# Kernel optimization log

Measured on AMD Instinct MI355X. Metric: run time of the kernel, lower is better.

## Reference

```python
import jax, jax.numpy as jnp
import numpy as np

T, BS, N = 256, 512, 2048
FUDGE = 1e-4


def setup_inputs() -> dict:
    key = jax.random.key(0)
    ks = jax.random.split(key, 6)
    f32 = jnp.float32
    return {
        "noises": jax.random.normal(ks[0], (T, BS), f32) * 0.1,  # per-step process noise [T, bs]
        "ys": jax.random.normal(ks[1], (T,), f32),               # per-step scalar targets
        "qs": jax.random.normal(ks[2], (T,), f32),               # per-step scalar context input
        "z_biases": jax.random.normal(ks[3], (N,), f32),         # random-feature bias directions
        "w_in": jax.random.normal(ks[4], (N,), f32),             # random input weights
        "w_inq": jax.random.normal(ks[5], (N,), f32),            # random q-input weights
        # scalar learned params (legacy init values)
        "log_learning_rate": jnp.array(-6.0, f32),
        "log_learning_rate_decay": jnp.array(0.0, f32),
        "sigma_b": jnp.array(0.1, f32),
        "output_scale": jnp.array(1.0, f32),
        "u_feedback_scale": jnp.array(1.0, f32),
        "log_weight_decay": jnp.array(-0.001, f32),
        "q_scale": jnp.array(1.0, f32),
        "tauqlpf_m1": jnp.array(-1.0, f32),
        "tauylpf_m1": jnp.array(-1.0, f32),
    }


def _forward(noises, ys, qs, z_biases, w_in, w_inq,
             log_learning_rate, log_learning_rate_decay, sigma_b,
             output_scale, u_feedback_scale, log_weight_decay, q_scale,
             tauqlpf_m1, tauylpf_m1):
    bs = noises.shape[1]
    n = w_in.shape[0]
    softplus = lambda v: jnp.log1p(jnp.exp(v))
    biases = sigma_b * z_biases                    # [n]
    lr0 = jnp.exp(log_learning_rate)               # scalar
    tauq = 1.0 + softplus(tauqlpf_m1)
    tauy = 1.0 + softplus(tauylpf_m1)
    wd = jnp.exp(log_weight_decay)                 # tie_lr_weight_decay=False -> scalar decay
    lr_decay_rate = jnp.exp(log_learning_rate_decay)

    def step(carry, inp):
        w_out, u, e, lr_mult, qlp, ylp = carry
        y, noise_x, q = inp
        qlp = (1.0 - tauq) * qlp + tauq * q
        q_in = w_inq * (q_scale * qlp)             # [n]
        x = u * u_feedback_scale + e + noise_x     # noise injected at node 'x'; [bs]
        h = jax.nn.relu(biases[None, :] + x[:, None] * w_in[None, :] + q_in[None, :])  # [bs, n]
        u = jnp.einsum('kj,kj->k', w_out, h)       # [bs]
        a_mean = output_scale * u                  # [bs]
        # y observed every step (no None/NaN branch)
        ylp = (1.0 - tauy) * ylp + tauy * y
        e = ylp - u                                # [bs]
        lr = lr0 * lr_mult                         # [bs]
        dw = e[:, None] * h * lr[:, None]          # [bs, n]
        w_out = w_out + dw
        norms = jnp.sqrt(FUDGE + jnp.sum(dw * dw, axis=1))
        lr_mult = lr_mult * jnp.exp(-lr_decay_rate * norms)
        w_out = wd * w_out
        return (w_out, u, e, lr_mult, qlp, ylp), a_mean

    init = (jnp.zeros((bs, n), noises.dtype),
            jnp.zeros((bs,), noises.dtype),
            jnp.zeros((bs,), noises.dtype),
            jnp.ones((bs,), noises.dtype),
            jnp.zeros((), noises.dtype),
            jnp.zeros((), noises.dtype))
    _, a_means = jax.lax.scan(step, init, (ys, noises, qs))
    return a_means  # [T, bs]


def reference(noises, ys, qs, z_biases, w_in, w_inq,
              log_learning_rate, log_learning_rate_decay, sigma_b,
              output_scale, u_feedback_scale, log_weight_decay, q_scale,
              tauqlpf_m1, tauylpf_m1):
    return _forward(noises, ys, qs, z_biases, w_in, w_inq,
                    log_learning_rate, log_learning_rate_decay, sigma_b,
                    output_scale, u_feedback_scale, log_weight_decay, q_scale,
                    tauqlpf_m1, tauylpf_m1)
```

## Files before the change

kernel.cpp:

```cpp
#include <hip/hip_runtime.h>
#include <math.h>
#include <stdint.h>

#define T_STEPS 256
#define BS      512
#define N       2048
#define BLOCK   256
#define FUDGE   1e-4f

__global__ __launch_bounds__(BLOCK, 2)
void legacy_elbo_scan_kernel(
    const float* __restrict__ noises,
    const float* __restrict__ ys,
    const float* __restrict__ qs,
    const float* __restrict__ z_biases,
    const float* __restrict__ w_in,
    const float* __restrict__ w_inq,
    const float* __restrict__ p_llr,
    const float* __restrict__ p_llrd,
    const float* __restrict__ p_sigb,
    const float* __restrict__ p_oscale,
    const float* __restrict__ p_ufs,
    const float* __restrict__ p_lwd,
    const float* __restrict__ p_qscale,
    const float* __restrict__ p_tauq,
    const float* __restrict__ p_tauy,
    float* __restrict__ out)
{
    const int tid = threadIdx.x;
    const int blk = blockIdx.x;

    __shared__ float red_lds[16];
    if (tid < 16) red_lds[tid] = 0.0f;
    __syncthreads();

    const float sigb    = p_sigb[0];
    const float lr0     = expf(p_llr[0]);
    const float lr_decay= expf(p_llrd[0]);
    const float wd      = expf(p_lwd[0]);
    const float rwd     = 1.0f / wd;
    const float tauq    = 1.0f + log1pf(expf(p_tauq[0]));
    const float tauy    = 1.0f + log1pf(expf(p_tauy[0]));
    const float omtq    = 1.0f - tauq;
    const float omty    = 1.0f - tauy;
    const float qscale  = p_qscale[0];
    const float ufs     = p_ufs[0];
    const float oscale  = p_oscale[0];
    const float nld2    = -lr_decay * 1.4426950408889634f;

    const float* nzp = noises + blk;
    const int    ovo = blk * 4;

    asm volatile(
        "v_lshrrev_b32 v3, 6, %[vtid]\n\t"
        "v_lshlrev_b32 v4, 3, v3\n\t"
        "v_and_b32 v7, 63, %[vtid]\n\t"
        "v_cmp_eq_u32 vcc, 63, v7\n\t"
        "s_mov_b64 s[74:75], vcc\n\t"
        "v_cmp_eq_u32 vcc, 0, %[vtid]\n\t"
        "s_mov_b64 s[76:77], vcc\n\t"
        "v_mov_b32 v5, 0\n\t"
        "v_lshlrev_b32 v1, 4, %[vtid]\n\t"
        "v_add_u32 v2, 0x1000, v1\n\t"
        "global_load_dwordx4 v[40:43], v1, %[pzb]\n\t"
        "global_load_dwordx4 v[44:47], v2, %[pzb]\n\t"
        "global_load_dwordx4 v[48:51], v1, %[pwi]\n\t"
        "global_load_dwordx4 v[52:55], v2, %[pwi]\n\t"
        "global_load_dwordx4 v[56:59], v1, %[pwq]\n\t"
        "global_load_dwordx4 v[60:63], v2, %[pwq]\n\t"
        "s_waitcnt vmcnt(0)\n\t"
        "v_mul_f32 v40, %[osg], v40\n\t"  "v_mul_f32 v41, %[osg], v41\n\t"
        "v_mul_f32 v42, %[osg], v42\n\t"  "v_mul_f32 v43, %[osg], v43\n\t"
        "v_mul_f32 v44, %[osg], v44\n\t"  "v_mul_f32 v45, %[osg], v45\n\t"
        "v_mul_f32 v46, %[osg], v46\n\t"  "v_mul_f32 v47, %[osg], v47\n\t"
        "v_mov_b32 v64, 0\n\t" "v_mov_b32 v65, 0\n\t" "v_mov_b32 v66, 0\n\t" "v_mov_b32 v67, 0\n\t"
        "v_mov_b32 v68, 0\n\t" "v_mov_b32 v69, 0\n\t" "v_mov_b32 v70, 0\n\t" "v_mov_b32 v71, 0\n\t"
        "v_mov_b32 v20, 0\n\t" "v_mov_b32 v21, 0\n\t" "v_mov_b32 v22, 0\n\t" "v_mov_b32 v23, 0\n\t"
        "v_mov_b32 v24, 1.0\n\t" "v_mov_b32 v25, 1.0\n\t" "v_mov_b32 v26, 1.0\n\t"
        "v_mov_b32 v6, %[ovo]\n\t"
        "s_mov_b32 s60, 0\n\t"
        "s_mov_b32 s61, 12\n\t"
        "s_mov_b32 s62, 0x1800\n\t"
        "s_load_dword s66, %[pys], 0x0\n\t"
        "s_load_dword s67, %[pqs], 0x0\n\t"
        "s_load_dword s68, %[pnz], 0x0\n\t"
        "s_load_dword s69, %[pys], 0x4\n\t"
        "s_load_dword s70, %[pqs], 0x4\n\t"
        "s_load_dword s71, %[pnz], 0x800\n\t"
        "s_load_dword s50, %[pys], 0x8\n\t"
        "s_load_dword s51, %[pqs], 0x8\n\t"
        "s_load_dword s52, %[pnz], 0x1000\n\t"
        "s_waitcnt lgkmcnt(0)\n\t"
        "Lelbo3:\n\t"
        "v_mov_b32 v30, s67\n\t"
        "v_mul_f32 v20, %[omq], v20\n\t"
        "v_fmac_f32 v20, %[otq], v30\n\t"
        "v_mul_f32 v10, %[oq], v20\n\t"
        "v_mov_b32 v11, v10\n\t"
        "v_mov_b32 v8, s68\n\t"
        "v_add_f32 v8, v23, v8\n\t"
        "v_fmac_f32 v8, %[ouf], v22\n\t"
        "v_mov_b32 v9, v8\n\t"
        "v_mov_b32 v12, 0\n\t" "v_mov_b32 v13, 0\n\t"
        "v_mov_b32 v14, 0\n\t" "v_mov_b32 v15, 0\n\t"
        "v_pk_fma_f32 v[72:73], v[10:11], v[56:57], v[40:41]\n\t"
        "v_pk_fma_f32 v[74:75], v[10:11], v[58:59], v[42:43]\n\t"
        "v_pk_fma_f32 v[76:77], v[10:11], v[60:61], v[44:45]\n\t"
        "v_pk_fma_f32 v[78:79], v[10:11], v[62:63], v[46:47]\n\t"
        "v_pk_fma_f32 v[72:73], v[8:9], v[48:49], v[72:73]\n\t"
        "v_pk_fma_f32 v[74:75], v[8:9], v[50:51], v[74:75]\n\t"
        "v_pk_fma_f32 v[76:77], v[8:9], v[52:53], v[76:77]\n\t"
        "v_pk_fma_f32 v[78:79], v[8:9], v[54:55], v[78:79]\n\t"
        "v_max_f32 v72, 0, v72\n\t" "v_max_f32 v73, 0, v73\n\t"
        "v_max_f32 v74, 0, v74\n\t" "v_max_f32 v75, 0, v75\n\t"
        "v_max_f32 v76, 0, v76\n\t" "v_max_f32 v77, 0, v77\n\t"
        "v_max_f32 v78, 0, v78\n\t" "v_max_f32 v79, 0, v79\n\t"
        "v_pk_fma_f32 v[12:13], v[64:65], v[72:73], v[12:13]\n\t"
        "v_pk_fma_f32 v[14:15], v[72:73], v[72:73], v[14:15]\n\t"
        "v_pk_fma_f32 v[12:13], v[66:67], v[74:75], v[12:13]\n\t"
        "v_pk_fma_f32 v[14:15], v[74:75], v[74:75], v[14:15]\n\t"
        "v_pk_fma_f32 v[12:13], v[68:69], v[76:77], v[12:13]\n\t"
        "v_pk_fma_f32 v[14:15], v[76:77], v[76:77], v[14:15]\n\t"
        "v_pk_fma_f32 v[12:13], v[70:71], v[78:79], v[12:13]\n\t"
        "v_pk_fma_f32 v[14:15], v[78:79], v[78:79], v[14:15]\n\t"
        "v_add_f32 v12, v12, v13\n\t"
        "v_add_f32 v14, v14, v15\n\t"
        "s_nop 1\n\t"
        "v_mov_b32_dpp v30, v12 row_shr:1 row_mask:0xf bank_mask:0xf\n\t"
        "v_mov_b32_dpp v31, v14 row_shr:1 row_mask:0xf bank_mask:0xf\n\t"
        "v_add_f32 v12, v12, v30\n\t"
        "v_add_f32 v14, v14, v31\n\t"
        "s_nop 0\n\t"
        "v_mov_b32_dpp v30, v12 row_shr:2 row_mask:0xf bank_mask:0xf\n\t"
        "v_mov_b32_dpp v31, v14 row_shr:2 row_mask:0xf bank_mask:0xf\n\t"
        "v_add_f32 v12, v12, v30\n\t"
        "v_add_f32 v14, v14, v31\n\t"
        "s_nop 0\n\t"
        "v_mov_b32_dpp v30, v12 row_shr:4 row_mask:0xf bank_mask:0xf\n\t"
        "v_mov_b32_dpp v31, v14 row_shr:4 row_mask:0xf bank_mask:0xf\n\t"
        "v_add_f32 v12, v12, v30\n\t"
        "v_add_f32 v14, v14, v31\n\t"
        "s_nop 0\n\t"
        "v_mov_b32_dpp v30, v12 row_shr:8 row_mask:0xf bank_mask:0xf\n\t"
        "v_mov_b32_dpp v31, v14 row_shr:8 row_mask:0xf bank_mask:0xf\n\t"
        "v_add_f32 v12, v12, v30\n\t"
        "v_add_f32 v14, v14, v31\n\t"
        "s_nop 0\n\t"
        "v_mov_b32_dpp v30, v12 row_bcast:15 row_mask:0xf bank_mask:0xf\n\t"
        "v_mov_b32_dpp v31, v14 row_bcast:15 row_mask:0xf bank_mask:0xf\n\t"
        "v_add_f32 v12, v12, v30\n\t"
        "v_add_f32 v14, v14, v31\n\t"
        "s_nop 0\n\t"
        "v_mov_b32_dpp v30, v12 row_bcast:31 row_mask:0xf bank_mask:0xf\n\t"
        "v_mov_b32_dpp v31, v14 row_bcast:31 row_mask:0xf bank_mask:0xf\n\t"
        "v_add_f32 v12, v12, v30\n\t"
        "v_add_f32 v14, v14, v31\n\t"
        "s_nop 1\n\t"
        "s_and_saveexec_b64 s[72:73], s[74:75]\n\t"
        "ds_write2_b32 v4, v12, v14 offset0:0 offset1:1\n\t"
        "s_mov_b64 exec, s[72:73]\n\t"
        "s_waitcnt lgkmcnt(0)\n\t"
        "s_barrier\n\t"
        "ds_read_b128 v[32:35], v5\n\t"
        "ds_read_b128 v[36:39], v5 offset:16\n\t"
        "v_mov_b32 v30, s66\n\t"
        "v_mul_f32 v21, %[omy], v21\n\t"
        "v_fmac_f32 v21, %[oty], v30\n\t"
        "v_xor_b32 v4, 32, v4\n\t"
        "v_xor_b32 v5, 32, v5\n\t"
        "s_mov_b32 s66, s69\n\t"
        "s_mov_b32 s67, s70\n\t"
        "s_mov_b32 s68, s71\n\t"
        "s_mov_b32 s69, s50\n\t"
        "s_mov_b32 s70, s51\n\t"
        "s_mov_b32 s71, s52\n\t"
        "s_add_u32 s60, s60, 1\n\t"
        "s_waitcnt lgkmcnt(0)\n\t"
        "v_pk_add_f32 v[32:33], v[32:33], v[34:35]\n\t"
        "v_pk_add_f32 v[36:37], v[36:37], v[38:39]\n\t"
        "v_pk_add_f32 v[32:33], v[32:33], v[36:37]\n\t"
        "v_mul_f32 v22, v25, v32\n\t"
        "v_mul_f32 v30, %[oos], v22\n\t"
        "s_and_saveexec_b64 s[72:73], s[76:77]\n\t"
        "global_store_dword v6, v30, %[pou]\n\t"
        "s_mov_b64 exec, s[72:73]\n\t"
        "v_add_u32 v6, 0x800, v6\n\t"
        "v_sub_f32 v23, v21, v22\n\t"
        "v_mul_f32 v27, %[olr], v23\n\t"
        "v_mul_f32 v27, v27, v24\n\t"
        "v_mul_f32 v28, v27, v26\n\t"
        "v_mov_b32 v29, v28\n\t"
        "s_load_dword s50, %[pys], s61\n\t"
        "s_load_dword s51, %[pqs], s61\n\t"
        "s_load_dword s52, %[pnz], s62\n\t"
        "s_add_u32 s61, s61, 4\n\t"
        "s_min_u32 s61, s61, 0x3fc\n\t"
        "s_add_u32 s62, s62, 0x800\n\t"
        "s_min_u32 s62, s62, 0x7f800\n\t"
        "v_pk_fma_f32 v[64:65], v[28:29], v[72:73], v[64:65]\n\t"
        "v_pk_fma_f32 v[66:67], v[28:29], v[74:75], v[66:67]\n\t"
        "v_pk_fma_f32 v[68:69], v[28:29], v[76:77], v[68:69]\n\t"
        "v_pk_fma_f32 v[70:71], v[28:29], v[78:79], v[70:71]\n\t"
        "v_mul_f32 v30, v27, v27\n\t"
        "v_mul_f32 v30, v33, v30\n\t"
        "v_add_f32 v30, 0x38d1b717, v30\n\t"
        "v_sqrt_f32 v30, v30\n\t"
        "s_nop 1\n\t"
        "v_mul_f32 v30, %[ond], v30\n\t"
        "v_exp_f32 v30, v30\n\t"
        "s_nop 1\n\t"
        "v_mul_f32 v24, v24, v30\n\t"
        "v_mul_f32 v25, %[owd], v25\n\t"
        "v_mul_f32 v26, %[orw], v26\n\t"
        "s_cmp_lt_u32 s60, 0x100\n\t"
        "s_cbranch_scc1 Lelbo3\n\t"
        "s_waitcnt vmcnt(0)\n\t"
        :
        : [pys]"s"(ys), [pqs]"s"(qs), [pnz]"s"(nzp), [pou]"s"(out),
          [pzb]"s"(z_biases), [pwi]"s"(w_in), [pwq]"s"(w_inq),
          [vtid]"v"(tid), [ovo]"v"(ovo),
          [osg]"v"(sigb), [otq]"v"(tauq), [omq]"v"(omtq),
          [oty]"v"(tauy), [omy]"v"(omty), [oq]"v"(qscale),
          [ouf]"v"(ufs), [olr]"v"(lr0), [owd]"v"(wd), [orw]"v"(rwd),
          [oos]"v"(oscale), [ond]"v"(nld2)
        : "memory", "scc", "vcc",
          "s50","s51","s52",
          "s60","s61","s62","s63","s64","s65","s66","s67","s68","s69",
          "s70","s71","s72","s73","s74","s75","s76","s77",
          "v1","v2","v3","v4","v5","v6","v7","v8","v9","v10","v11",
          "v12","v13","v14","v15","v16","v17","v18","v19","v20","v21",
          "v22","v23","v24","v25","v26","v27","v28","v29","v30","v31",
          "v32","v33","v34","v35","v36","v37","v38","v39","v40","v41",
          "v42","v43","v44","v45","v46","v47","v48","v49","v50","v51",
          "v52","v53","v54","v55","v56","v57","v58","v59","v60","v61",
          "v62","v63","v64","v65","v66","v67","v68","v69","v70","v71",
          "v72","v73","v74","v75","v76","v77","v78","v79"
    );
}

extern "C" void kernel_launch(void* const* d_in, const int* in_sizes, int n_in,
                              void* d_out, int out_size, void* d_ws, size_t ws_size,
                              hipStream_t stream) {
    (void)in_sizes; (void)n_in; (void)d_ws; (void)ws_size; (void)out_size;
    const float* noises   = (const float*)d_in[0];
    const float* ys       = (const float*)d_in[1];
    const float* qs       = (const float*)d_in[2];
    const float* z_biases = (const float*)d_in[3];
    const float* w_in     = (const float*)d_in[4];
    const float* w_inq    = (const float*)d_in[5];
    const float* llr      = (const float*)d_in[6];
    const float* llrd     = (const float*)d_in[7];
    const float* sigb     = (const float*)d_in[8];
    const float* oscale   = (const float*)d_in[9];
    const float* ufs      = (const float*)d_in[10];
    const float* lwd      = (const float*)d_in[11];
    const float* qscale   = (const float*)d_in[12];
    const float* tauq     = (const float*)d_in[13];
    const float* tauy     = (const float*)d_in[14];
    float* out = (float*)d_out;

    hipLaunchKernelGGL(legacy_elbo_scan_kernel, dim3(BS), dim3(BLOCK), 64, stream,
                       noises, ys, qs, z_biases, w_in, w_inq,
                       llr, llrd, sigb, oscale, ufs, lwd, qscale, tauq, tauy,
                       out);
}
```

Baseline: 189.2 us.

## Process two batch rows per block, sharing barriers and q-input precompute

Each block now handles two batch elements, so the grid halves to 256 blocks. The per-step w_in/z_bias/w_inq registers and the q-dependent pre-activation are shared across both rows. Reductions for both rows are interleaved in a single DPP chain and one LDS exchange, which halves barriers per element and gives more independent instructions to hide latency. The qlp/ylp and x updates are precomputed and pipelined off the critical path. In exchange it uses more VGPRs and only 256 blocks, which may underfill a 256-CU device.

```diff
diff --git a/kernel.cpp b/kernel.cpp
--- a/kernel.cpp
+++ b/kernel.cpp
@@ -8,7 +8,7 @@
 #define BLOCK   256
 #define FUDGE   1e-4f
 
-__global__ __launch_bounds__(BLOCK, 2)
+__global__ __launch_bounds__(BLOCK)
 void legacy_elbo_scan_kernel(
     const float* __restrict__ noises,
     const float* __restrict__ ys,
@@ -30,8 +30,8 @@
     const int tid = threadIdx.x;
     const int blk = blockIdx.x;
 
-    __shared__ float red_lds[16];
-    if (tid < 16) red_lds[tid] = 0.0f;
+    __shared__ float red_lds[32];
+    if (tid < 32) red_lds[tid] = 0.0f;
     __syncthreads();
 
     const float sigb    = p_sigb[0];
@@ -44,16 +44,16 @@
     const float omtq    = 1.0f - tauq;
     const float omty    = 1.0f - tauy;
     const float qscale  = p_qscale[0];
-    const float ufs     = p_ufs[0];
+    const float ufsm1   = p_ufs[0] - 1.0f;
     const float oscale  = p_oscale[0];
     const float nld2    = -lr_decay * 1.4426950408889634f;
 
-    const float* nzp = noises + blk;
-    const int    ovo = blk * 4;
+    const float* nzp = noises + 2 * blk;
+    const int    ovo = blk * 8;
 
     asm volatile(
         "v_lshrrev_b32 v3, 6, %[vtid]\n\t"
-        "v_lshlrev_b32 v4, 3, v3\n\t"
+        "v_lshlrev_b32 v4, 4, v3\n\t"
         "v_and_b32 v7, 63, %[vtid]\n\t"
         "v_cmp_eq_u32 vcc, 63, v7\n\t"
         "s_mov_b64 s[74:75], vcc\n\t"
@@ -62,171 +62,256 @@
         "v_mov_b32 v5, 0\n\t"
         "v_lshlrev_b32 v1, 4, %[vtid]\n\t"
         "v_add_u32 v2, 0x1000, v1\n\t"
-        "global_load_dwordx4 v[40:43], v1, %[pzb]\n\t"
-        "global_load_dwordx4 v[44:47], v2, %[pzb]\n\t"
-        "global_load_dwordx4 v[48:51], v1, %[pwi]\n\t"
-        "global_load_dwordx4 v[52:55], v2, %[pwi]\n\t"
-        "global_load_dwordx4 v[56:59], v1, %[pwq]\n\t"
-        "global_load_dwordx4 v[60:63], v2, %[pwq]\n\t"
-        "s_waitcnt vmcnt(0)\n\t"
-        "v_mul_f32 v40, %[osg], v40\n\t"  "v_mul_f32 v41, %[osg], v41\n\t"
-        "v_mul_f32 v42, %[osg], v42\n\t"  "v_mul_f32 v43, %[osg], v43\n\t"
-        "v_mul_f32 v44, %[osg], v44\n\t"  "v_mul_f32 v45, %[osg], v45\n\t"
-        "v_mul_f32 v46, %[osg], v46\n\t"  "v_mul_f32 v47, %[osg], v47\n\t"
+        "global_load_dwordx4 v[56:59], v1, %[pzb]\n\t"
+        "global_load_dwordx4 v[60:63], v2, %[pzb]\n\t"
+        "global_load_dwordx4 v[40:43], v1, %[pwi]\n\t"
+        "global_load_dwordx4 v[44:47], v2, %[pwi]\n\t"
+        "global_load_dwordx4 v[48:51], v1, %[pwq]\n\t"
+        "global_load_dwordx4 v[52:55], v2, %[pwq]\n\t"
+        "s_load_dword s66, %[pys], 0x0\n\t"
+        "s_load_dword s67, %[pqs], 0x0\n\t"
+        "s_load_dwordx2 s[68:69], %[pnz], 0x0\n\t"
+        "s_load_dword s70, %[pys], 0x4\n\t"
+        "s_load_dword s71, %[pqs], 0x4\n\t"
+        "s_load_dwordx2 s[54:55], %[pnz], 0x800\n\t"
+        "s_load_dword s50, %[pys], 0x8\n\t"
+        "s_load_dword s51, %[pqs], 0x8\n\t"
+        "s_load_dwordx2 s[52:53], %[pnz], 0x1000\n\t"
+        "s_mov_b32 s61, 12\n\t"
+        "s_mov_b32 s62, 0x1800\n\t"
+        "s_mov_b32 s60, 0\n\t"
+        "s_waitcnt vmcnt(0) lgkmcnt(0)\n\t"
+        "v_mul_f32 v56, %[osg], v56\n\t" "v_mul_f32 v57, %[osg], v57\n\t"
+        "v_mul_f32 v58, %[osg], v58\n\t" "v_mul_f32 v59, %[osg], v59\n\t"
+        "v_mul_f32 v60, %[osg], v60\n\t" "v_mul_f32 v61, %[osg], v61\n\t"
+        "v_mul_f32 v62, %[osg], v62\n\t" "v_mul_f32 v63, %[osg], v63\n\t"
         "v_mov_b32 v64, 0\n\t" "v_mov_b32 v65, 0\n\t" "v_mov_b32 v66, 0\n\t" "v_mov_b32 v67, 0\n\t"
         "v_mov_b32 v68, 0\n\t" "v_mov_b32 v69, 0\n\t" "v_mov_b32 v70, 0\n\t" "v_mov_b32 v71, 0\n\t"
-        "v_mov_b32 v20, 0\n\t" "v_mov_b32 v21, 0\n\t" "v_mov_b32 v22, 0\n\t" "v_mov_b32 v23, 0\n\t"
-        "v_mov_b32 v24, 1.0\n\t" "v_mov_b32 v25, 1.0\n\t" "v_mov_b32 v26, 1.0\n\t"
+        "v_mov_b32 v96, 0\n\t" "v_mov_b32 v97, 0\n\t" "v_mov_b32 v98, 0\n\t" "v_mov_b32 v99, 0\n\t"
+        "v_mov_b32 v100, 0\n\t" "v_mov_b32 v101, 0\n\t" "v_mov_b32 v102, 0\n\t" "v_mov_b32 v103, 0\n\t"
+        "v_mov_b32 v105, 0\n\t"
+        "v_mov_b32 v108, 1.0\n\t" "v_mov_b32 v109, 1.0\n\t"
+        "v_mov_b32 v110, 1.0\n\t" "v_mov_b32 v111, 1.0\n\t"
         "v_mov_b32 v6, %[ovo]\n\t"
-        "s_mov_b32 s60, 0\n\t"
-        "s_mov_b32 s61, 12\n\t"
-        "s_mov_b32 s62, 0x1800\n\t"
-        "s_load_dword s66, %[pys], 0x0\n\t"
-        "s_load_dword s67, %[pqs], 0x0\n\t"
-        "s_load_dword s68, %[pnz], 0x0\n\t"
-        "s_load_dword s69, %[pys], 0x4\n\t"
-        "s_load_dword s70, %[pqs], 0x4\n\t"
-        "s_load_dword s71, %[pnz], 0x800\n\t"
-        "s_load_dword s50, %[pys], 0x8\n\t"
-        "s_load_dword s51, %[pqs], 0x8\n\t"
-        "s_load_dword s52, %[pnz], 0x1000\n\t"
-        "s_waitcnt lgkmcnt(0)\n\t"
-        "Lelbo3:\n\t"
-        "v_mov_b32 v30, s67\n\t"
-        "v_mul_f32 v20, %[omq], v20\n\t"
-        "v_fmac_f32 v20, %[otq], v30\n\t"
-        "v_mul_f32 v10, %[oq], v20\n\t"
-        "v_mov_b32 v11, v10\n\t"
-        "v_mov_b32 v8, s68\n\t"
-        "v_add_f32 v8, v23, v8\n\t"
-        "v_fmac_f32 v8, %[ouf], v22\n\t"
-        "v_mov_b32 v9, v8\n\t"
-        "v_mov_b32 v12, 0\n\t" "v_mov_b32 v13, 0\n\t"
-        "v_mov_b32 v14, 0\n\t" "v_mov_b32 v15, 0\n\t"
-        "v_pk_fma_f32 v[72:73], v[10:11], v[56:57], v[40:41]\n\t"
-        "v_pk_fma_f32 v[74:75], v[10:11], v[58:59], v[42:43]\n\t"
-        "v_pk_fma_f32 v[76:77], v[10:11], v[60:61], v[44:45]\n\t"
-        "v_pk_fma_f32 v[78:79], v[10:11], v[62:63], v[46:47]\n\t"
-        "v_pk_fma_f32 v[72:73], v[8:9], v[48:49], v[72:73]\n\t"
-        "v_pk_fma_f32 v[74:75], v[8:9], v[50:51], v[74:75]\n\t"
-        "v_pk_fma_f32 v[76:77], v[8:9], v[52:53], v[76:77]\n\t"
-        "v_pk_fma_f32 v[78:79], v[8:9], v[54:55], v[78:79]\n\t"
-        "v_max_f32 v72, 0, v72\n\t" "v_max_f32 v73, 0, v73\n\t"
-        "v_max_f32 v74, 0, v74\n\t" "v_max_f32 v75, 0, v75\n\t"
-        "v_max_f32 v76, 0, v76\n\t" "v_max_f32 v77, 0, v77\n\t"
-        "v_max_f32 v78, 0, v78\n\t" "v_max_f32 v79, 0, v79\n\t"
-        "v_pk_fma_f32 v[12:13], v[64:65], v[72:73], v[12:13]\n\t"
-        "v_pk_fma_f32 v[14:15], v[72:73], v[72:73], v[14:15]\n\t"
-        "v_pk_fma_f32 v[12:13], v[66:67], v[74:75], v[12:13]\n\t"
-        "v_pk_fma_f32 v[14:15], v[74:75], v[74:75], v[14:15]\n\t"
-        "v_pk_fma_f32 v[12:13], v[68:69], v[76:77], v[12:13]\n\t"
-        "v_pk_fma_f32 v[14:15], v[76:77], v[76:77], v[14:15]\n\t"
-        "v_pk_fma_f32 v[12:13], v[70:71], v[78:79], v[12:13]\n\t"
-        "v_pk_fma_f32 v[14:15], v[78:79], v[78:79], v[14:15]\n\t"
-        "v_add_f32 v12, v12, v13\n\t"
-        "v_add_f32 v14, v14, v15\n\t"
+        "v_mul_f32 v104, s67, %[otq]\n\t"
+        "v_mul_f32 v12, v104, %[oq]\n\t"
+        "v_mov_b32 v13, v12\n\t"
+        "v_pk_fma_f32 v[80:81], v[12:13], v[48:49], v[56:57]\n\t"
+        "v_pk_fma_f32 v[82:83], v[12:13], v[50:51], v[58:59]\n\t"
+        "v_pk_fma_f32 v[84:85], v[12:13], v[52:53], v[60:61]\n\t"
+        "v_pk_fma_f32 v[86:87], v[12:13], v[54:55], v[62:63]\n\t"
+        "v_mov_b32 v8, s68\n\t"  "v_mov_b32 v9, v8\n\t"
+        "v_mov_b32 v10, s69\n\t" "v_mov_b32 v11, v10\n\t"
+        "Lelbo5:\n\t"
+        "v_pk_fma_f32 v[72:73], v[8:9], v[40:41], v[80:81]\n\t"
+        "v_pk_fma_f32 v[88:89], v[10:11], v[40:41], v[80:81]\n\t"
+        "v_pk_fma_f32 v[74:75], v[8:9], v[42:43], v[82:83]\n\t"
+        "v_pk_fma_f32 v[90:91], v[10:11], v[42:43], v[82:83]\n\t"
+        "v_pk_fma_f32 v[76:77], v[8:9], v[44:45], v[84:85]\n\t"
+        "v_pk_fma_f32 v[92:93], v[10:11], v[44:45], v[84:85]\n\t"
+        "v_pk_fma_f32 v[78:79], v[8:9], v[46:47], v[86:87]\n\t"
+        "v_pk_fma_f32 v[94:95], v[10:11], v[46:47], v[86:87]\n\t"
+        "v_max_f32 v72, 0, v72\n\t" "v_max_f32 v88, 0, v88\n\t"
+        "v_max_f32 v73, 0, v73\n\t" "v_max_f32 v89, 0, v89\n\t"
+        "v_max_f32 v74, 0, v74\n\t" "v_max_f32 v90, 0, v90\n\t"
+        "v_max_f32 v75, 0, v75\n\t" "v_max_f32 v91, 0, v91\n\t"
+        "v_max_f32 v76, 0, v76\n\t" "v_max_f32 v92, 0, v92\n\t"
+        "v_max_f32 v77, 0, v77\n\t" "v_max_f32 v93, 0, v93\n\t"
+        "v_max_f32 v78, 0, v78\n\t" "v_max_f32 v94, 0, v94\n\t"
+        "v_max_f32 v79, 0, v79\n\t" "v_max_f32 v95, 0, v95\n\t"
+        "v_pk_mul_f32 v[16:17], v[64:65], v[72:73]\n\t"
+        "v_pk_mul_f32 v[24:25], v[96:97], v[88:89]\n\t"
+        "v_pk_mul_f32 v[18:19], v[66:67], v[74:75]\n\t"
+        "v_pk_mul_f32 v[26:27], v[98:99], v[90:91]\n\t"
+        "v_pk_mul_f32 v[20:21], v[68:69], v[76:77]\n\t"
+        "v_pk_mul_f32 v[28:29], v[100:101], v[92:93]\n\t"
+        "v_pk_mul_f32 v[22:23], v[70:71], v[78:79]\n\t"
+        "v_pk_mul_f32 v[30:31], v[102:103], v[94:95]\n\t"
+        "v_pk_add_f32 v[16:17], v[16:17], v[18:19]\n\t"
+        "v_pk_add_f32 v[24:25], v[24:25], v[26:27]\n\t"
+        "v_pk_add_f32 v[20:21], v[20:21], v[22:23]\n\t"
+        "v_pk_add_f32 v[28:29], v[28:29], v[30:31]\n\t"
+        "v_pk_add_f32 v[16:17], v[16:17], v[20:21]\n\t"
+        "v_pk_add_f32 v[24:25], v[24:25], v[28:29]\n\t"
+        "v_add_f32 v16, v16, v17\n\t"
+        "v_add_f32 v24, v24, v25\n\t"
+        "v_pk_mul_f32 v[18:19], v[72:73], v[72:73]\n\t"
+        "v_pk_mul_f32 v[26:27], v[88:89], v[88:89]\n\t"
+        "v_pk_mul_f32 v[20:21], v[74:75], v[74:75]\n\t"
+        "v_pk_mul_f32 v[28:29], v[90:91], v[90:91]\n\t"
+        "v_pk_mul_f32 v[22:23], v[76:77], v[76:77]\n\t"
+        "v_pk_mul_f32 v[30:31], v[92:93], v[92:93]\n\t"
+        "v_pk_mul_f32 v[36:37], v[78:79], v[78:79]\n\t"
+        "v_pk_mul_f32 v[38:39], v[94:95], v[94:95]\n\t"
+        "v_pk_add_f32 v[18:19], v[18:19], v[20:21]\n\t"
+        "v_pk_add_f32 v[26:27], v[26:27], v[28:29]\n\t"
+        "v_pk_add_f32 v[22:23], v[22:23], v[36:37]\n\t"
+        "v_pk_add_f32 v[30:31], v[30:31], v[38:39]\n\t"
+        "v_pk_add_f32 v[18:19], v[18:19], v[22:23]\n\t"
+        "v_pk_add_f32 v[26:27], v[26:27], v[30:31]\n\t"
+        "v_add_f32 v18, v18, v19\n\t"
+        "v_add_f32 v26, v26, v27\n\t"
         "s_nop 1\n\t"
-        "v_mov_b32_dpp v30, v12 row_shr:1 row_mask:0xf bank_mask:0xf\n\t"
-        "v_mov_b32_dpp v31, v14 row_shr:1 row_mask:0xf bank_mask:0xf\n\t"
-        "v_add_f32 v12, v12, v30\n\t"
-        "v_add_f32 v14, v14, v31\n\t"
-        "s_nop 0\n\t"
-        "v_mov_b32_dpp v30, v12 row_shr:2 row_mask:0xf bank_mask:0xf\n\t"
-        "v_mov_b32_dpp v31, v14 row_shr:2 row_mask:0xf bank_mask:0xf\n\t"
-        "v_add_f32 v12, v12, v30\n\t"
-        "v_add_f32 v14, v14, v31\n\t"
-        "s_nop 0\n\t"
-        "v_mov_b32_dpp v30, v12 row_shr:4 row_mask:0xf bank_mask:0xf\n\t"
-        "v_mov_b32_dpp v31, v14 row_shr:4 row_mask:0xf bank_mask:0xf\n\t"
-        "v_add_f32 v12, v12, v30\n\t"
-        "v_add_f32 v14, v14, v31\n\t"
-        "s_nop 0\n\t"
-        "v_mov_b32_dpp v30, v12 row_shr:8 row_mask:0xf bank_mask:0xf\n\t"
-        "v_mov_b32_dpp v31, v14 row_shr:8 row_mask:0xf bank_mask:0xf\n\t"
-        "v_add_f32 v12, v12, v30\n\t"
-        "v_add_f32 v14, v14, v31\n\t"
-        "s_nop 0\n\t"
-        "v_mov_b32_dpp v30, v12 row_bcast:15 row_mask:0xf bank_mask:0xf\n\t"
-        "v_mov_b32_dpp v31, v14 row_bcast:15 row_mask:0xf bank_mask:0xf\n\t"
-        "v_add_f32 v12, v12, v30\n\t"
-        "v_add_f32 v14, v14, v31\n\t"
-        "s_nop 0\n\t"
-        "v_mov_b32_dpp v30, v12 row_bcast:31 row_mask:0xf bank_mask:0xf\n\t"
-        "v_mov_b32_dpp v31, v14 row_bcast:31 row_mask:0xf bank_mask:0xf\n\t"
-        "v_add_f32 v12, v12, v30\n\t"
-        "v_add_f32 v14, v14, v31\n\t"
+        "v_mov_b32_dpp v32, v16 row_shr:1 row_mask:0xf bank_mask:0xf\n\t"
+        "v_mov_b32_dpp v33, v18 row_shr:1 row_mask:0xf bank_mask:0xf\n\t"
+        "v_mov_b32_dpp v34, v24 row_shr:1 row_mask:0xf bank_mask:0xf\n\t"
+        "v_mov_b32_dpp v35, v26 row_shr:1 row_mask:0xf bank_mask:0xf\n\t"
+        "v_add_f32 v16, v16, v32\n\t"
+        "v_add_f32 v18, v18, v33\n\t"
+        "v_add_f32 v24, v24, v34\n\t"
+        "v_add_f32 v26, v26, v35\n\t"
+        "v_mov_b32_dpp v32, v16 row_shr:2 row_mask:0xf bank_mask:0xf\n\t"
+        "v_mov_b32_dpp v33, v18 row_shr:2 row_mask:0xf bank_mask:0xf\n\t"
+        "v_mov_b32_dpp v34, v24 row_shr:2 row_mask:0xf bank_mask:0xf\n\t"
+        "v_mov_b32_dpp v35, v26 row_shr:2 row_mask:0xf bank_mask:0xf\n\t"
+        "v_add_f32 v16, v16, v32\n\t"
+        "v_add_f32 v18, v18, v33\n\t"
+        "v_add_f32 v24, v24, v34\n\t"
+        "v_add_f32 v26, v26, v35\n\t"
+        "v_mov_b32_dpp v32, v16 row_shr:4 row_mask:0xf bank_mask:0xf\n\t"
+        "v_mov_b32_dpp v33, v18 row_shr:4 row_mask:0xf bank_mask:0xf\n\t"
+        "v_mov_b32_dpp v34, v24 row_shr:4 row_mask:0xf bank_mask:0xf\n\t"
+        "v_mov_b32_dpp v35, v26 row_shr:4 row_mask:0xf bank_mask:0xf\n\t"
+        "v_add_f32 v16, v16, v32\n\t"
+        "v_add_f32 v18, v18, v33\n\t"
+        "v_add_f32 v24, v24, v34\n\t"
+        "v_add_f32 v26, v26, v35\n\t"
+        "v_mov_b32_dpp v32, v16 row_shr:8 row_mask:0xf bank_mask:0xf\n\t"
+        "v_mov_b32_dpp v33, v18 row_shr:8 row_mask:0xf bank_mask:0xf\n\t"
+        "v_mov_b32_dpp v34, v24 row_shr:8 row_mask:0xf bank_mask:0xf\n\t"
+        "v_mov_b32_dpp v35, v26 row_shr:8 row_mask:0xf bank_mask:0xf\n\t"
+        "v_add_f32 v16, v16, v32\n\t"
+        "v_add_f32 v18, v18, v33\n\t"
+        "v_add_f32 v24, v24, v34\n\t"
+        "v_add_f32 v26, v26, v35\n\t"
+        "v_mov_b32_dpp v32, v16 row_bcast:15 row_mask:0xf bank_mask:0xf\n\t"
+        "v_mov_b32_dpp v33, v18 row_bcast:15 row_mask:0xf bank_mask:0xf\n\t"
+        "v_mov_b32_dpp v34, v24 row_bcast:15 row_mask:0xf bank_mask:0xf\n\t"
+        "v_mov_b32_dpp v35, v26 row_bcast:15 row_mask:0xf bank_mask:0xf\n\t"
+        "v_add_f32 v16, v16, v32\n\t"
+        "v_add_f32 v18, v18, v33\n\t"
+        "v_add_f32 v24, v24, v34\n\t"
+        "v_add_f32 v26, v26, v35\n\t"
+        "v_mov_b32_dpp v32, v16 row_bcast:31 row_mask:0xf bank_mask:0xf\n\t"
+        "v_mov_b32_dpp v33, v18 row_bcast:31 row_mask:0xf bank_mask:0xf\n\t"
+        "v_mov_b32_dpp v34, v24 row_bcast:31 row_mask:0xf bank_mask:0xf\n\t"
+        "v_mov_b32_dpp v35, v26 row_bcast:31 row_mask:0xf bank_mask:0xf\n\t"
+        "v_add_f32 v16, v16, v32\n\t"
+        "v_add_f32 v18, v18, v33\n\t"
+        "v_add_f32 v24, v24, v34\n\t"
+        "v_add_f32 v26, v26, v35\n\t"
         "s_nop 1\n\t"
+        "v_mov_b32 v36, v16\n\t"
+        "v_mov_b32 v37, v18\n\t"
+        "v_mov_b32 v38, v24\n\t"
+        "v_mov_b32 v39, v26\n\t"
         "s_and_saveexec_b64 s[72:73], s[74:75]\n\t"
-        "ds_write2_b32 v4, v12, v14 offset0:0 offset1:1\n\t"
+        "ds_write_b128 v4, v[36:39]\n\t"
         "s_mov_b64 exec, s[72:73]\n\t"
         "s_waitcnt lgkmcnt(0)\n\t"
         "s_barrier\n\t"
-        "ds_read_b128 v[32:35], v5\n\t"
-        "ds_read_b128 v[36:39], v5 offset:16\n\t"
-        "v_mov_b32 v30, s66\n\t"
-        "v_mul_f32 v21, %[omy], v21\n\t"
-        "v_fmac_f32 v21, %[oty], v30\n\t"
-        "v_xor_b32 v4, 32, v4\n\t"
-        "v_xor_b32 v5, 32, v5\n\t"
-        "s_mov_b32 s66, s69\n\t"
-        "s_mov_b32 s67, s70\n\t"
-        "s_mov_b32 s68, s71\n\t"
-        "s_mov_b32 s69, s50\n\t"
-        "s_mov_b32 s70, s51\n\t"
-        "s_mov_b32 s71, s52\n\t"
+        "ds_read_b128 v[16:19], v5\n\t"
+        "ds_read_b128 v[20:23], v5 offset:16\n\t"
+        "ds_read_b128 v[24:27], v5 offset:32\n\t"
+        "ds_read_b128 v[28:31], v5 offset:48\n\t"
+        "v_mul_f32 v104, %[omq], v104\n\t"
+        "v_fmac_f32 v104, s71, %[otq]\n\t"
+        "v_mul_f32 v12, v104, %[oq]\n\t"
+        "v_mov_b32 v13, v12\n\t"
+        "v_pk_fma_f32 v[80:81], v[12:13], v[48:49], v[56:57]\n\t"
+        "v_pk_fma_f32 v[82:83], v[12:13], v[50:51], v[58:59]\n\t"
+        "v_pk_fma_f32 v[84:85], v[12:13], v[52:53], v[60:61]\n\t"
+        "v_pk_fma_f32 v[86:87], v[12:13], v[54:55], v[62:63]\n\t"
+        "v_mul_f32 v105, %[omy], v105\n\t"
+        "v_fmac_f32 v105, s66, %[oty]\n\t"
+        "v_add_f32 v112, s54, v105\n\t"
+        "v_add_f32 v113, s55, v105\n\t"
+        "v_mul_f32 v114, %[olr], v108\n\t"
+        "v_mul_f32 v115, %[olr], v109\n\t"
+        "v_xor_b32 v4, 64, v4\n\t"
+        "v_xor_b32 v5, 64, v5\n\t"
+        "s_mov_b32 s66, s70\n\t"
+        "s_mov_b32 s67, s71\n\t"
+        "s_mov_b32 s68, s54\n\t"
+        "s_mov_b32 s69, s55\n\t"
+        "s_mov_b32 s70, s50\n\t"
+        "s_mov_b32 s71, s51\n\t"
+        "s_mov_b32 s54, s52\n\t"
+        "s_mov_b32 s55, s53\n\t"
         "s_add_u32 s60, s60, 1\n\t"
         "s_waitcnt lgkmcnt(0)\n\t"
-        "v_pk_add_f32 v[32:33], v[32:33], v[34:35]\n\t"
-        "v_pk_add_f32 v[36:37], v[36:37], v[38:39]\n\t"
-        "v_pk_add_f32 v[32:33], v[32:33], v[36:37]\n\t"
-        "v_mul_f32 v22, v25, v32\n\t"
-        "v_mul_f32 v30, %[oos], v22\n\t"
-        "s_and_saveexec_b64 s[72:73], s[76:77]\n\t"
-        "global_store_dword v6, v30, %[pou]\n\t"
-        "s_mov_b64 exec, s[72:73]\n\t"
-        "v_add_u32 v6, 0x800, v6\n\t"
-        "v_sub_f32 v23, v21, v22\n\t"
-        "v_mul_f32 v27, %[olr], v23\n\t"
-        "v_mul_f32 v27, v27, v24\n\t"
-        "v_mul_f32 v28, v27, v26\n\t"
-        "v_mov_b32 v29, v28\n\t"
+        "v_pk_add_f32 v[16:17], v[16:17], v[20:21]\n\t"
+        "v_pk_add_f32 v[18:19], v[18:19], v[22:23]\n\t"
+        "v_pk_add_f32 v[24:25], v[24:25], v[28:29]\n\t"
+        "v_pk_add_f32 v[26:27], v[26:27], v[30:31]\n\t"
+        "v_pk_add_f32 v[16:17], v[16:17], v[24:25]\n\t"
+        "v_pk_add_f32 v[18:19], v[18:19], v[26:27]\n\t"
         "s_load_dword s50, %[pys], s61\n\t"
         "s_load_dword s51, %[pqs], s61\n\t"
-        "s_load_dword s52, %[pnz], s62\n\t"
+        "s_load_dwordx2 s[52:53], %[pnz], s62\n\t"
         "s_add_u32 s61, s61, 4\n\t"
         "s_min_u32 s61, s61, 0x3fc\n\t"
         "s_add_u32 s62, s62, 0x800\n\t"
         "s_min_u32 s62, s62, 0x7f800\n\t"
-        "v_pk_fma_f32 v[64:65], v[28:29], v[72:73], v[64:65]\n\t"
-        "v_pk_fma_f32 v[66:67], v[28:29], v[74:75], v[66:67]\n\t"
-        "v_pk_fma_f32 v[68:69], v[28:29], v[76:77], v[68:69]\n\t"
-        "v_pk_fma_f32 v[70:71], v[28:29], v[78:79], v[70:71]\n\t"
-        "v_mul_f32 v30, v27, v27\n\t"
-        "v_mul_f32 v30, v33, v30\n\t"
+        "v_mul_f32 v106, v16, v110\n\t"
+        "v_mul_f32 v107, v18, v110\n\t"
+        "v_mul_f32 v36, %[oos], v106\n\t"
+        "v_mul_f32 v37, %[oos], v107\n\t"
+        "s_and_saveexec_b64 s[72:73], s[76:77]\n\t"
+        "global_store_dwordx2 v6, v[36:37], %[pou]\n\t"
+        "s_mov_b64 exec, s[72:73]\n\t"
+        "v_add_u32 v6, 0x800, v6\n\t"
+        "v_fma_f32 v8, %[oum], v106, v112\n\t"
+        "v_mov_b32 v9, v8\n\t"
+        "v_fma_f32 v10, %[oum], v107, v113\n\t"
+        "v_mov_b32 v11, v10\n\t"
+        "v_sub_f32 v38, v105, v106\n\t"
+        "v_sub_f32 v39, v105, v107\n\t"
+        "v_mul_f32 v38, v114, v38\n\t"
+        "v_mul_f32 v39, v115, v39\n\t"
+        "v_mul_f32 v14, v38, v111\n\t"
+        "v_mov_b32 v15, v14\n\t"
+        "v_mul_f32 v34, v39, v111\n\t"
+        "v_mov_b32 v35, v34\n\t"
+        "v_mul_f32 v30, v38, v38\n\t"
+        "v_mul_f32 v31, v39, v39\n\t"
+        "v_mul_f32 v30, v17, v30\n\t"
+        "v_mul_f32 v31, v19, v31\n\t"
         "v_add_f32 v30, 0x38d1b717, v30\n\t"
+        "v_add_f32 v31, 0x38d1b717, v31\n\t"
         "v_sqrt_f32 v30, v30\n\t"
-        "s_nop 1\n\t"
+        "v_sqrt_f32 v31, v31\n\t"
+        "v_pk_fma_f32 v[64:65], v[14:15], v[72:73], v[64:65]\n\t"
+        "v_pk_fma_f32 v[96:97], v[34:35], v[88:89], v[96:97]\n\t"
+        "v_pk_fma_f32 v[66:67], v[14:15], v[74:75], v[66:67]\n\t"
+        "v_pk_fma_f32 v[98:99], v[34:35], v[90:91], v[98:99]\n\t"
         "v_mul_f32 v30, %[ond], v30\n\t"
+        "v_mul_f32 v31, %[ond], v31\n\t"
         "v_exp_f32 v30, v30\n\t"
-        "s_nop 1\n\t"
-        "v_mul_f32 v24, v24, v30\n\t"
-        "v_mul_f32 v25, %[owd], v25\n\t"
-        "v_mul_f32 v26, %[orw], v26\n\t"
+        "v_exp_f32 v31, v31\n\t"
+        "v_pk_fma_f32 v[68:69], v[14:15], v[76:77], v[68:69]\n\t"
+        "v_pk_fma_f32 v[100:101], v[34:35], v[92:93], v[100:101]\n\t"
+        "v_pk_fma_f32 v[70:71], v[14:15], v[78:79], v[70:71]\n\t"
+        "v_pk_fma_f32 v[102:103], v[34:35], v[94:95], v[102:103]\n\t"
+        "v_mul_f32 v110, %[owd], v110\n\t"
+        "v_mul_f32 v111, %[orw], v111\n\t"
+        "v_mul_f32 v108, v108, v30\n\t"
+        "v_mul_f32 v109, v109, v31\n\t"
         "s_cmp_lt_u32 s60, 0x100\n\t"
-        "s_cbranch_scc1 Lelbo3\n\t"
-        "s_waitcnt vmcnt(0)\n\t"
+        "s_cbranch_scc1 Lelbo5\n\t"
+        "s_waitcnt vmcnt(0) lgkmcnt(0)\n\t"
         :
         : [pys]"s"(ys), [pqs]"s"(qs), [pnz]"s"(nzp), [pou]"s"(out),
           [pzb]"s"(z_biases), [pwi]"s"(w_in), [pwq]"s"(w_inq),
           [vtid]"v"(tid), [ovo]"v"(ovo),
           [osg]"v"(sigb), [otq]"v"(tauq), [omq]"v"(omtq),
           [oty]"v"(tauy), [omy]"v"(omty), [oq]"v"(qscale),
-          [ouf]"v"(ufs), [olr]"v"(lr0), [owd]"v"(wd), [orw]"v"(rwd),
+          [oum]"v"(ufsm1), [olr]"v"(lr0), [owd]"v"(wd), [orw]"v"(rwd),
           [oos]"v"(oscale), [ond]"v"(nld2)
         : "memory", "scc", "vcc",
-          "s50","s51","s52",
-          "s60","s61","s62","s63","s64","s65","s66","s67","s68","s69",
-          "s70","s71","s72","s73","s74","s75","s76","s77",
+          "s50","s51","s52","s53","s54","s55",
+          "s60","s61","s62","s66","s67","s68","s69","s70","s71",
+          "s72","s73","s74","s75","s76","s77",
           "v1","v2","v3","v4","v5","v6","v7","v8","v9","v10","v11",
           "v12","v13","v14","v15","v16","v17","v18","v19","v20","v21",
           "v22","v23","v24","v25","v26","v27","v28","v29","v30","v31",
@@ -234,7 +319,11 @@
           "v42","v43","v44","v45","v46","v47","v48","v49","v50","v51",
           "v52","v53","v54","v55","v56","v57","v58","v59","v60","v61",
           "v62","v63","v64","v65","v66","v67","v68","v69","v70","v71",
-          "v72","v73","v74","v75","v76","v77","v78","v79"
+          "v72","v73","v74","v75","v76","v77","v78","v79","v80","v81",
+          "v82","v83","v84","v85","v86","v87","v88","v89","v90","v91",
+          "v92","v93","v94","v95","v96","v97","v98","v99","v100","v101",
+          "v102","v103","v104","v105","v106","v107","v108","v109","v110",
+          "v111","v112","v113","v114","v115"
     );
 }
 
@@ -259,7 +348,8 @@
     const float* tauy     = (const float*)d_in[14];
     float* out = (float*)d_out;
 
-    hipLaunchKernelGGL(legacy_elbo_scan_kernel, dim3(BS), dim3(BLOCK), 64, stream,
+    hipLaunchKernelGGL(legacy_elbo_scan_kernel, dim3(BS / 2), dim3(BLOCK), 128,
+                       stream,
                        noises, ys, qs, z_biases, w_in, w_inq,
                        llr, llrd, sigb, oscale, ufs, lwd, qscale, tauq, tauy,
                        out);
```

New measurement: 205.8 us. 8.8% more time.
